# Kernel optimization log

Hardware: AMD Instinct MI355X
Metric: run time of the kernel (lower is better)

## Reference

```python
import jax, jax.numpy as jnp
import numpy as np

B, S, DM = 8, 1024, 1024
H, DH = 16, 64  # num_heads, per-head dim (q=k=v=r)
SCALE = 64 ** 1 / 2  # faithful to source: d_k**1/2 == d_k/2 == 32.0


def setup_inputs() -> dict:
    key = jax.random.key(0)
    ks = jax.random.split(key, 13)
    std = 1.0 / np.sqrt(DM)
    def lin(k):
        kw, kb = jax.random.split(k)
        W = jax.random.uniform(kw, (DM, H * DH), jnp.float32, -std, std)
        b = jax.random.uniform(kb, (H * DH,), jnp.float32, -std, std)
        return W, b
    Wq, bq = lin(ks[0]); Wk, bk = lin(ks[1]); Wv, bv = lin(ks[2]); Wr, br = lin(ks[3])
    Wo = jax.random.uniform(ks[4], (H * DH, DM), jnp.float32, -std, std)
    bo = jax.random.uniform(ks[5], (DM,), jnp.float32, -std, std)
    return {
        "value": jax.random.normal(ks[6], (B, S, DM), jnp.float32),
        "key": jax.random.normal(ks[7], (B, S, DM), jnp.float32),
        "query": jax.random.normal(ks[8], (B, S, DM), jnp.float32),
        "Wq": Wq, "bq": bq, "Wk": Wk, "bk": bk,
        "Wv": Wv, "bv": bv, "Wr": Wr, "br": br,
        "Wo": Wo, "bo": bo,
    }


def reference(value, key, query, Wq, bq, Wk, bk, Wv, bv, Wr, br, Wo, bo):
    b = query.shape[0]
    # projections -> [b, s, h, d] -> [b, h, s, d]
    q = (query @ Wq + bq).reshape(b, -1, H, DH).transpose(0, 2, 1, 3)
    k = (key @ Wk + bk).reshape(b, -1, H, DH).transpose(0, 2, 1, 3)
    v = (value @ Wv + bv).reshape(b, -1, H, DH).transpose(0, 2, 1, 3)
    r = (query @ Wr + br).reshape(b, -1, H, DH).transpose(0, 2, 1, 3)
    energy = jnp.einsum('bhid,bhjd->bhij', q, k)
    attn = jax.nn.softmax(energy / SCALE, axis=-1)
    ctx = jnp.einsum('bhjd,bhij->bhid', v, attn)
    gated = (ctx * r).transpose(0, 2, 1, 3)  # R-gating, back to [b, s, h, d]
    out = gated.reshape(b, -1, H * DH) @ Wo + bo
    return out
```

## Files before the change

### kernel.cpp

```cpp
#include <hip/hip_runtime.h>
#include <stdint.h>

#define B_ 8
#define S_ 1024
#define DM_ 1024
#define H_ 16
#define DH_ 64
#define M_ (B_*S_)

typedef unsigned short u16;
typedef unsigned int u32;
typedef __attribute__((ext_vector_type(8))) short bf16x8;
typedef __attribute__((ext_vector_type(4))) float f32x4;

__device__ __forceinline__ u16 f2bf(float f){
  union { float f; u32 u; } x; x.f = f;
  u32 r = x.u + 0x7fffu + ((x.u >> 16) & 1u);
  return (u16)(r >> 16);
}
__device__ __forceinline__ float bf2f(u16 u){
  union { u32 u; float f; } x; x.u = ((u32)u) << 16; return x.f;
}
__device__ __forceinline__ u32 cvtpk(float lo, float hi){
  u32 r; asm("v_cvt_pk_bf16_f32 %0, %1, %2" : "=v"(r) : "v"(lo), "v"(hi)); return r;
}
__device__ __forceinline__ void gload16(const void* g, void* l){
  __builtin_amdgcn_global_load_lds((const __attribute__((address_space(1))) void*)g,
                                   (__attribute__((address_space(3))) void*)l, 16, 0, 0);
}

__global__ void k_cvt_act(const float* __restrict__ v, const float* __restrict__ k,
                          const float* __restrict__ q, u16* __restrict__ vb,
                          u16* __restrict__ kb, u16* __restrict__ qb){
  int z = blockIdx.y;
  const float* src = (z == 0) ? v : (z == 1) ? k : q;
  u16* dst = (z == 0) ? vb : (z == 1) ? kb : qb;
  size_t i = ((size_t)blockIdx.x * blockDim.x + threadIdx.x) * 8;
  float4 a = *(const float4*)(src + i);
  float4 b = *(const float4*)(src + i + 4);
  uint4 o;
  o.x = (u32)f2bf(a.x) | ((u32)f2bf(a.y) << 16);
  o.y = (u32)f2bf(a.z) | ((u32)f2bf(a.w) << 16);
  o.z = (u32)f2bf(b.x) | ((u32)f2bf(b.y) << 16);
  o.w = (u32)f2bf(b.z) | ((u32)f2bf(b.w) << 16);
  *(uint4*)(dst + i) = o;
}

__global__ void k_cvt_wt(const float* __restrict__ w0, const float* __restrict__ w1,
                         const float* __restrict__ w2, const float* __restrict__ w3,
                         const float* __restrict__ w4,
                         u16* __restrict__ wall, u16* __restrict__ wot){
  __shared__ float tile[32][33];
  int z = blockIdx.z;
  const float* src = (z==0)?w0:(z==1)?w1:(z==2)?w2:(z==3)?w3:w4;
  u16* dst = (z<4) ? (wall + (size_t)z * 1048576) : wot;
  int n0 = blockIdx.x * 32, k0 = blockIdx.y * 32;
  int tx = threadIdx.x, ty = threadIdx.y;
#pragma unroll
  for (int i=0;i<4;i++) tile[ty+8*i][tx] = src[(size_t)(k0+ty+8*i)*DM_ + n0+tx];
  __syncthreads();
#pragma unroll
  for (int i=0;i<4;i++) dst[(size_t)(n0+ty+8*i)*DM_ + k0+tx] = f2bf(tile[tx][ty+8*i]);
}

__global__ __launch_bounds__(512, 2) void k_proj8(const u16* __restrict__ qb, const u16* __restrict__ kb,
                                                  const u16* __restrict__ vb, const u16* __restrict__ wall,
                                                  const float* __restrict__ bqp, const float* __restrict__ brp,
                                                  const float* __restrict__ bkp, const float* __restrict__ bvp,
                                                  u16* __restrict__ qpj, u16* __restrict__ rpj,
                                                  u16* __restrict__ kpj, u16* __restrict__ vtg){
  extern __shared__ u16 smem[];
  u16* As = smem;
  u16* Bs = smem + 32768;
  const int tid = threadIdx.x;
  const int w = tid >> 6, l = tid & 63, g = l >> 4, s = l & 15;
  const int wr = w >> 2, wc = w & 3;
  const int m0 = blockIdx.x << 8;
  const int ng0 = blockIdx.y << 8;
  const int chunk = ng0 >> 10;
  const u16* A = (chunk < 2) ? qb : (chunk == 2) ? kb : vb;

  u32 offA[2][2], offB[2][2];
#pragma unroll
  for (int h=0; h<2; h++)
#pragma unroll
    for (int i2=0; i2<2; i2++){
      int c = tid + i2*512; int rw = c >> 3, sl = c & 7;
      offA[h][i2] = (u32)((m0  + h*128 + rw) << 10) + ((sl ^ (rw & 7)) << 3);
      offB[h][i2] = (u32)((ng0 + h*128 + rw) << 10) + ((sl ^ (rw & 7)) << 3);
    }
  const u16* pA[2]; const u16* pB[2];
#pragma unroll
  for (int ks=0; ks<2; ks++){
    pA[ks] = &As[(wr*128 + s)*64 + (((ks*4+g) ^ (s & 7)) << 3)];
    pB[ks] = &Bs[(wc*64  + s)*64 + (((ks*4+g) ^ (s & 7)) << 3)];
  }

  f32x4 acc[8][4];
#pragma unroll
  for (int i=0;i<8;i++)
#pragma unroll
    for (int j=0;j<4;j++) acc[i][j] = (f32x4){0.f,0.f,0.f,0.f};

#define PSTAGE_A(buf, TCE, h) do { \
    gload16(Ak + offA[h][0] + (TCE), &As[(buf)*16384 + (h)*8192 + (w*64)*8]); \
    gload16(Ak + offA[h][1] + (TCE), &As[(buf)*16384 + (h)*8192 + (512 + w*64)*8]); \
  } while(0)

#define PSTAGE_B(buf, TCE, h) do { \
    gload16(Wk + offB[h][0] + (TCE), &Bs[(buf)*16384 + (h)*8192 + (w*64)*8]); \
    gload16(Wk + offB[h][1] + (TCE), &Bs[(buf)*16384 + (h)*8192 + (512 + w*64)*8]); \
  } while(0)

#define PLOADA(cb, mh) do { \
    _Pragma("unroll") for (int mi2=0; mi2<4; mi2++) \
    _Pragma("unroll") for (int ks=0; ks<2; ks++) \
      af[mi2][ks] = *(const bf16x8*)(pA[ks] + (cb)*16384 + (mh)*4096 + mi2*1024); \
    } while(0)

#define PLOADB(dst, cb, nh) do { \
    _Pragma("unroll") for (int ni2=0; ni2<2; ni2++) \
    _Pragma("unroll") for (int ks=0; ks<2; ks++) \
      dst[ni2][ks] = *(const bf16x8*)(pB[ks] + (cb)*16384 + (nh)*2048 + ni2*1024); \
    } while(0)

#define PMFMA(mh, nh, bfr) do { \
    _Pragma("unroll") for (int mi2=0; mi2<4; mi2++) \
    _Pragma("unroll") for (int ni2=0; ni2<2; ni2++) \
    _Pragma("unroll") for (int ks=0; ks<2; ks++) \
      acc[(mh)*4+mi2][(nh)*2+ni2] = __builtin_amdgcn_mfma_f32_16x16x32_bf16( \
          af[mi2][ks], bfr[ni2][ks], acc[(mh)*4+mi2][(nh)*2+ni2], 0, 0, 0); \
    } while(0)

#define BAR   __builtin_amdgcn_s_barrier()
#define PRIO1 __builtin_amdgcn_s_setprio(1)
#define PRIO0 __builtin_amdgcn_s_setprio(0)
#define VMC(N) asm volatile("s_waitcnt vmcnt(" #N ")" ::: "memory")

  {
    const u16* Ak = A;  const u16* Wk = wall;
    PSTAGE_A(0, 0, 0); PSTAGE_A(0, 0, 1); PSTAGE_B(0, 0, 0); PSTAGE_B(0, 0, 1);
    PSTAGE_B(1, 64, 0); PSTAGE_B(1, 64, 1);
  }
  VMC(4);
  BAR;

#pragma unroll 1
  for (int it = 0; it < 8; ++it){
    const u16* Ak = A + it*128;
    const u16* Wk = wall + it*128;
    const bool pre = (it < 7);
    {
      bf16x8 af[4][2], bf0[2][2], bf1[2][2];
      PSTAGE_A(1, 64, 0);
      PLOADA(0, 0); PLOADB(bf0, 0, 0);
      PRIO1; PMFMA(0, 0, bf0); PRIO0; BAR;
      PSTAGE_A(1, 64, 1);
      PLOADB(bf1, 0, 1);
      PRIO1; PMFMA(0, 1, bf1); PRIO0;
      VMC(8);
      BAR;
      if (pre) PSTAGE_B(0, 128, 0);
      PLOADA(0, 1);
      PRIO1; PMFMA(1, 1, bf1); PRIO0; BAR;
      if (pre) PSTAGE_B(0, 128, 1);
      PRIO1; PMFMA(1, 0, bf0); PRIO0;
      if (it == 7) VMC(0); else VMC(6);
      BAR;
    }
    {
      bf16x8 af[4][2], bf0[2][2], bf1[2][2];
      if (pre) PSTAGE_A(0, 128, 0);
      PLOADA(1, 0); PLOADB(bf0, 1, 0);
      PRIO1; PMFMA(0, 0, bf0); PRIO0; BAR;
      if (pre) PSTAGE_A(0, 128, 1);
      PLOADB(bf1, 1, 1);
      PRIO1; PMFMA(0, 1, bf1); PRIO0;
      VMC(8);
      BAR;
      if (pre) PSTAGE_B(1, 192, 0);
      PLOADA(1, 1);
      PRIO1; PMFMA(1, 1, bf1); PRIO0; BAR;
      if (pre) PSTAGE_B(1, 192, 1);
      PRIO1; PMFMA(1, 0, bf0); PRIO0;
      VMC(6);
      BAR;
    }
  }

  const float* bias = (chunk==0)?bqp:(chunk==1)?brp:(chunk==2)?bkp:bvp;
  u16* outp = (chunk==0)?qpj:(chunk==1)?rpj:kpj;
#pragma unroll
  for (int ni=0; ni<4; ni++){
    int cg = ng0 + wc*64 + ni*16 + s;
    int col = cg & 1023;
    float bv = bias[col];
#pragma unroll
    for (int mi=0; mi<8; mi++){
      int row = m0 + wr*128 + mi*16 + g*4;
      if (chunk == 3){
        union { short4 v; u16 e[4]; } pk2;
#pragma unroll
        for (int r=0;r<4;r++) pk2.e[r] = f2bf(acc[mi][ni][r] + bv);
        size_t vrow = ((size_t)(row >> 10) * 16 + (col >> 6)) * 64 + (col & 63);
        *(short4*)&vtg[(vrow << 10) + (row & 1023)] = pk2.v;
      } else {
#pragma unroll
        for (int r=0;r<4;r++)
          outp[((size_t)(row+r) << 10) + col] = f2bf(acc[mi][ni][r] + bv);
      }
    }
  }
#undef PSTAGE_A
#undef PSTAGE_B
#undef PLOADA
#undef PLOADB
#undef PMFMA
#undef BAR
#undef PRIO1
#undef PRIO0
#undef VMC
}

__global__ __launch_bounds__(256) void k_gemm_out(const u16* __restrict__ A, const u16* __restrict__ Bt,
                                                  const float* __restrict__ bias, float* __restrict__ Out){
  __shared__ u16 As[128*64];
  __shared__ u16 Bs[128*64];
  const int tid = threadIdx.x;
  const int w = tid >> 6, l = tid & 63, g = l >> 4, s = l & 15;
  const int wr = w >> 1, wc = w & 1;
  const int m0 = blockIdx.x << 7, n0 = blockIdx.y << 7;
  f32x4 acc[4][4];
#pragma unroll
  for (int i=0;i<4;i++)
#pragma unroll
    for (int j=0;j<4;j++) acc[i][j] = (f32x4){0.f,0.f,0.f,0.f};

  for (int k0 = 0; k0 < 1024; k0 += 64){
    __syncthreads();
#pragma unroll
    for (int i=0;i<4;i++){
      int c = tid + i*256;
      int m = c >> 3, slot = c & 7;
      gload16(A + ((size_t)(m0+m) << 10) + (k0 + ((slot ^ (m & 7)) << 3)),
              &As[(i*256 + w*64) * 8]);
    }
#pragma unroll
    for (int i=0;i<4;i++){
      int c = tid + i*256;
      int n = c >> 3, slot = c & 7;
      gload16(Bt + ((size_t)(n0+n) << 10) + (k0 + ((slot ^ (n & 7)) << 3)),
              &Bs[(i*256 + w*64) * 8]);
    }
    __syncthreads();
#pragma unroll
    for (int ks=0; ks<2; ks++){
      bf16x8 af[4], bfv[4];
#pragma unroll
      for (int mi=0;mi<4;mi++){
        int m = wr*64 + mi*16 + s;
        af[mi] = *(const bf16x8*)&As[m*64 + (((ks*4+g) ^ (s & 7)) << 3)];
      }
#pragma unroll
      for (int ni=0;ni<4;ni++){
        int n = wc*64 + ni*16 + s;
        bfv[ni] = *(const bf16x8*)&Bs[n*64 + (((ks*4+g) ^ (s & 7)) << 3)];
      }
#pragma unroll
      for (int mi=0;mi<4;mi++)
#pragma unroll
        for (int ni=0;ni<4;ni++)
          acc[mi][ni] = __builtin_amdgcn_mfma_f32_16x16x32_bf16(af[mi], bfv[ni], acc[mi][ni], 0, 0, 0);
    }
  }
#pragma unroll
  for (int ni=0;ni<4;ni++){
    int col = n0 + wc*64 + ni*16 + s;
    float bv = bias[col];
#pragma unroll
    for (int mi=0;mi<4;mi++){
      int row = m0 + wr*64 + mi*16 + g*4;
#pragma unroll
      for (int r=0;r<4;r++)
        Out[((size_t)(row+r) << 10) + col] = acc[mi][ni][r] + bv;
    }
  }
}

__global__ __launch_bounds__(512) void k_attn(const u16* __restrict__ qp, const u16* __restrict__ kp,
                                              const u16* __restrict__ vtg, const u16* __restrict__ rp,
                                              u16* __restrict__ gated){
  __shared__ u16 Ks[2][64*64];
  __shared__ u16 Vs[2][64*64];
  __shared__ u32 PsU[8*16*32];
  const int tid = threadIdx.x;
  const int w = tid >> 6, l = tid & 63, g = l >> 4, s = l & 15;
  const int bid = blockIdx.x;
  const int swz = (bid & 7) * 128 + (bid >> 3);
  const int bh = swz >> 3;
  const int q0 = (swz & 7) << 7;
  const int b = bh >> 4, h = bh & 15;
  const size_t base = ((size_t)b << 20);
  const int colh = h << 6;
  const float KL = 1.4426950408889634f / 32.0f;

  const size_t qoff = base + ((size_t)(q0 + w*16 + s) << 10) + colh;
  bf16x8 qf0 = *(const bf16x8*)(qp + qoff + g*8);
  bf16x8 qf1 = *(const bf16x8*)(qp + qoff + 32 + g*8);
  const size_t vbase = ((size_t)(b*16 + h)) << 16;

  u32* PsW = PsU + (w << 9);
  const int sx2 = s << 1;

  const int rr = tid >> 3, sl = tid & 7;
  const u32 koff = (u32)(rr << 10) + colh + ((sl ^ (rr & 7)) << 3);
  const u32 voff = (u32)(rr << 10) + ((sl ^ (rr & 7)) << 3);
  const u16* kbgl = kp + base;
  const u16* vbgl = vtg + vbase;

  float mrun = -1e30f, lsum = 0.f;
  f32x4 of[4];
#pragma unroll
  for (int d=0;d<4;d++) of[d] = (f32x4){0.f,0.f,0.f,0.f};

#define STAGE_KV(BUF, KV0) do { \
    gload16(kbgl + ((u32)(KV0) << 10) + koff, &Ks[BUF][(w*64)*8]); \
    gload16(vbgl + (KV0) + voff, &Vs[BUF][(w*64)*8]); \
  } while(0)

  STAGE_KV(0, 0);
  __syncthreads();

  int cur = 0;
  for (int t = 0; t < 16; t++){
    if (t < 15) STAGE_KV(cur ^ 1, (t+1) << 6);
    const u16* ksb = Ks[cur];
    const u16* vsb = Vs[cur];

    f32x4 e2[4];
#pragma unroll
    for (int sjf=0;sjf<4;sjf++){
      e2[sjf] = (f32x4){0.f,0.f,0.f,0.f};
      int sj = sjf*16 + s;
      bf16x8 kf0 = *(const bf16x8*)&ksb[sj*64 + ((g ^ (s & 7)) << 3)];
      e2[sjf] = __builtin_amdgcn_mfma_f32_16x16x32_bf16(kf0, qf0, e2[sjf], 0, 0, 0);
      bf16x8 kf1 = *(const bf16x8*)&ksb[sj*64 + (((4+g) ^ (s & 7)) << 3)];
      e2[sjf] = __builtin_amdgcn_mfma_f32_16x16x32_bf16(kf1, qf1, e2[sjf], 0, 0, 0);
    }
    float rm = fmaxf(fmaxf(e2[0][0], e2[0][1]), e2[0][2]);
    rm = fmaxf(fmaxf(rm, e2[0][3]), e2[1][0]);
    rm = fmaxf(fmaxf(rm, e2[1][1]), e2[1][2]);
    rm = fmaxf(fmaxf(rm, e2[1][3]), e2[2][0]);
    rm = fmaxf(fmaxf(rm, e2[2][1]), e2[2][2]);
    rm = fmaxf(fmaxf(rm, e2[2][3]), e2[3][0]);
    rm = fmaxf(fmaxf(rm, e2[3][1]), e2[3][2]);
    rm = fmaxf(rm, e2[3][3]);
    rm = fmaxf(rm, __shfl_xor(rm, 16, 64));
    rm = fmaxf(rm, __shfl_xor(rm, 32, 64));
    if (!__all(rm <= mrun + 177.0f)){
      float nm = fmaxf(mrun, rm);
      float alpha = __builtin_amdgcn_exp2f((mrun - nm) * KL);
      mrun = nm;
      lsum *= alpha;
      float ac[4];
#pragma unroll
      for (int r=0;r<4;r++) ac[r] = __shfl(alpha, g*4 + r, 64);
#pragma unroll
      for (int d=0; d<4; d++)
#pragma unroll
        for (int r=0;r<4;r++) of[d][r] *= ac[r];
    }

    const float mk = mrun * KL;
#pragma unroll
    for (int sjf=0;sjf<4;sjf++){
      float p0 = __builtin_amdgcn_exp2f(e2[sjf][0]*KL - mk);
      float p1 = __builtin_amdgcn_exp2f(e2[sjf][1]*KL - mk);
      float p2 = __builtin_amdgcn_exp2f(e2[sjf][2]*KL - mk);
      float p3 = __builtin_amdgcn_exp2f(e2[sjf][3]*KL - mk);
      lsum += (p0 + p1) + (p2 + p3);
      uint2 pk; pk.x = cvtpk(p0, p1); pk.y = cvtpk(p2, p3);
      int phys = (8*sjf + 2*g) ^ sx2;
      *reinterpret_cast<uint2*>(&PsW[(s << 5) + phys]) = pk;
    }
    union { u32 u[4]; bf16x8 v; } pa0, pa1;
    {
      uint2 r0 = *reinterpret_cast<const uint2*>(&PsW[(s << 5) + ((4*g    ) ^ sx2)]);
      uint2 r1 = *reinterpret_cast<const uint2*>(&PsW[(s << 5) + ((4*g + 2) ^ sx2)]);
      pa0.u[0] = r0.x; pa0.u[1] = r0.y; pa0.u[2] = r1.x; pa0.u[3] = r1.y;
      uint2 r2 = *reinterpret_cast<const uint2*>(&PsW[(s << 5) + ((16 + 4*g    ) ^ sx2)]);
      uint2 r3 = *reinterpret_cast<const uint2*>(&PsW[(s << 5) + ((16 + 4*g + 2) ^ sx2)]);
      pa1.u[0] = r2.x; pa1.u[1] = r2.y; pa1.u[2] = r3.x; pa1.u[3] = r3.y;
    }
#pragma unroll
    for (int df=0; df<4; df++){
      int d = df*16 + s;
      bf16x8 v0 = *(const bf16x8*)&vsb[d*64 + ((g ^ (s & 7)) << 3)];
      bf16x8 v1 = *(const bf16x8*)&vsb[d*64 + (((4+g) ^ (s & 7)) << 3)];
      of[df] = __builtin_amdgcn_mfma_f32_16x16x32_bf16(pa0.v, v0, of[df], 0, 0, 0);
      of[df] = __builtin_amdgcn_mfma_f32_16x16x32_bf16(pa1.v, v1, of[df], 0, 0, 0);
    }
    __syncthreads();
    cur ^= 1;
  }
#undef STAGE_KV

  lsum += __shfl_xor(lsum, 16, 64);
  lsum += __shfl_xor(lsum, 32, 64);
  float inv = 1.0f / lsum;
  float ic[4];
#pragma unroll
  for (int r=0;r<4;r++) ic[r] = __shfl(inv, g*4 + r, 64);
#pragma unroll
  for (int df=0; df<4; df++){
#pragma unroll
    for (int r=0;r<4;r++){
      size_t row = (size_t)(q0 + w*16 + g*4 + r);
      size_t idx = base + (row << 10) + colh + df*16 + s;
      float o = of[df][r] * ic[r];
      float rg = bf2f(rp[idx]);
      gated[idx] = f2bf(o * rg);
    }
  }
}

extern "C" void kernel_launch(void* const* d_in, const int* in_sizes, int n_in,
                              void* d_out, int out_size, void* d_ws, size_t ws_size,
                              hipStream_t stream){
  (void)in_sizes; (void)n_in; (void)out_size; (void)ws_size;
  const float* value = (const float*)d_in[0];
  const float* key   = (const float*)d_in[1];
  const float* query = (const float*)d_in[2];
  const float* Wq = (const float*)d_in[3];  const float* bq = (const float*)d_in[4];
  const float* Wk = (const float*)d_in[5];  const float* bk = (const float*)d_in[6];
  const float* Wv = (const float*)d_in[7];  const float* bv = (const float*)d_in[8];
  const float* Wr = (const float*)d_in[9];  const float* br = (const float*)d_in[10];
  const float* Wo = (const float*)d_in[11]; const float* bo = (const float*)d_in[12];

  char* ws = (char*)d_ws;
  const size_t MB = (size_t)1 << 20;
  u16* qb   = (u16*)(ws + 0*MB);
  u16* kb   = (u16*)(ws + 16*MB);
  u16* vb   = (u16*)(ws + 32*MB);
  u16* wall = (u16*)(ws + 48*MB);
  u16* wot  = (u16*)(ws + 56*MB);
  u16* qpj  = (u16*)(ws + 58*MB);
  u16* kpj  = (u16*)(ws + 74*MB);
  u16* vtg  = (u16*)(ws + 90*MB);
  u16* rpj  = (u16*)(ws + 106*MB);
  u16* gat  = qb;

  (void)hipFuncSetAttribute(reinterpret_cast<const void*>(&k_proj8),
                            hipFuncAttributeMaxDynamicSharedMemorySize, 131072);

  k_cvt_act<<<dim3(4096, 3), 256, 0, stream>>>(value, key, query, vb, kb, qb);
  k_cvt_wt<<<dim3(32, 32, 5), dim3(32, 8), 0, stream>>>(Wq, Wr, Wk, Wv, Wo, wall, wot);
  k_proj8<<<dim3(32, 16), 512, 131072, stream>>>(qb, kb, vb, wall, bq, br, bk, bv,
                                                 qpj, rpj, kpj, vtg);
  k_attn<<<1024, 512, 0, stream>>>(qpj, kpj, vtg, rpj, gat);
  k_gemm_out<<<dim3(64, 8), 256, 0, stream>>>(gat, wot, bo, (float*)d_out);
}
```

Measured before the change: 190.0 us.

## Software-pipeline LDS fragment loads ahead of MFMA phases in projection GEMM

Restructures the projection GEMM main loop so the LDS-to-register fragment loads for the next MFMA phase are issued before the current phase's MFMAs, using double sets of A/B fragment registers that persist across iterations. This is meant to hide LDS read latency behind matrix-core work instead of stalling on each load. It raises register pressure, which may reduce occupancy or cause spills, and it reorders waitcnt and barrier placement in a way that must stay correct against the global-to-LDS staging.

Measured after the change: 329.9 us. 1.74x slower.

```diff
diff --git a/kernel.cpp b/kernel.cpp
--- a/kernel.cpp
+++ b/kernel.cpp
@@ -112,10 +112,10 @@
     gload16(Wk + offB[h][1] + (TCE), &Bs[(buf)*16384 + (h)*8192 + (512 + w*64)*8]); \
   } while(0)
 
-#define PLOADA(cb, mh) do { \
+#define PLOADA(dst, cb, mh) do { \
     _Pragma("unroll") for (int mi2=0; mi2<4; mi2++) \
     _Pragma("unroll") for (int ks=0; ks<2; ks++) \
-      af[mi2][ks] = *(const bf16x8*)(pA[ks] + (cb)*16384 + (mh)*4096 + mi2*1024); \
+      dst[mi2][ks] = *(const bf16x8*)(pA[ks] + (cb)*16384 + (mh)*4096 + mi2*1024); \
     } while(0)
 
 #define PLOADB(dst, cb, nh) do { \
@@ -124,12 +124,12 @@
       dst[ni2][ks] = *(const bf16x8*)(pB[ks] + (cb)*16384 + (nh)*2048 + ni2*1024); \
     } while(0)
 
-#define PMFMA(mh, nh, bfr) do { \
+#define PMFMA(mh, nh, afr, bfr) do { \
     _Pragma("unroll") for (int mi2=0; mi2<4; mi2++) \
     _Pragma("unroll") for (int ni2=0; ni2<2; ni2++) \
     _Pragma("unroll") for (int ks=0; ks<2; ks++) \
       acc[(mh)*4+mi2][(nh)*2+ni2] = __builtin_amdgcn_mfma_f32_16x16x32_bf16( \
-          af[mi2][ks], bfr[ni2][ks], acc[(mh)*4+mi2][(nh)*2+ni2], 0, 0, 0); \
+          afr[mi2][ks], bfr[ni2][ks], acc[(mh)*4+mi2][(nh)*2+ni2], 0, 0, 0); \
     } while(0)
 
 #define BAR   __builtin_amdgcn_s_barrier()
@@ -137,6 +137,9 @@
 #define PRIO0 __builtin_amdgcn_s_setprio(0)
 #define VMC(N) asm volatile("s_waitcnt vmcnt(" #N ")" ::: "memory")
 
+  bf16x8 aX0[4][2], aX1[4][2], aY0[4][2], aY1[4][2];
+  bf16x8 bX0[2][2], bX1[2][2], bY0[2][2], bY1[2][2];
+
   {
     const u16* Ak = A;  const u16* Wk = wall;
     PSTAGE_A(0, 0, 0); PSTAGE_A(0, 0, 1); PSTAGE_B(0, 0, 0); PSTAGE_B(0, 0, 1);
@@ -144,48 +147,41 @@
   }
   VMC(4);
   BAR;
+  PLOADA(aX0, 0, 0); PLOADB(bX0, 0, 0);
 
 #pragma unroll 1
   for (int it = 0; it < 8; ++it){
     const u16* Ak = A + it*128;
     const u16* Wk = wall + it*128;
     const bool pre = (it < 7);
-    {
-      bf16x8 af[4][2], bf0[2][2], bf1[2][2];
-      PSTAGE_A(1, 64, 0);
-      PLOADA(0, 0); PLOADB(bf0, 0, 0);
-      PRIO1; PMFMA(0, 0, bf0); PRIO0; BAR;
-      PSTAGE_A(1, 64, 1);
-      PLOADB(bf1, 0, 1);
-      PRIO1; PMFMA(0, 1, bf1); PRIO0;
-      VMC(8);
-      BAR;
-      if (pre) PSTAGE_B(0, 128, 0);
-      PLOADA(0, 1);
-      PRIO1; PMFMA(1, 1, bf1); PRIO0; BAR;
-      if (pre) PSTAGE_B(0, 128, 1);
-      PRIO1; PMFMA(1, 0, bf0); PRIO0;
-      if (it == 7) VMC(0); else VMC(6);
-      BAR;
-    }
-    {
-      bf16x8 af[4][2], bf0[2][2], bf1[2][2];
-      if (pre) PSTAGE_A(0, 128, 0);
-      PLOADA(1, 0); PLOADB(bf0, 1, 0);
-      PRIO1; PMFMA(0, 0, bf0); PRIO0; BAR;
-      if (pre) PSTAGE_A(0, 128, 1);
-      PLOADB(bf1, 1, 1);
-      PRIO1; PMFMA(0, 1, bf1); PRIO0;
-      VMC(8);
-      BAR;
-      if (pre) PSTAGE_B(1, 192, 0);
-      PLOADA(1, 1);
-      PRIO1; PMFMA(1, 1, bf1); PRIO0; BAR;
-      if (pre) PSTAGE_B(1, 192, 1);
-      PRIO1; PMFMA(1, 0, bf0); PRIO0;
+    PSTAGE_A(1, 64, 0);
+    PLOADB(bX1, 0, 1);
+    PRIO1; PMFMA(0, 0, aX0, bX0); PRIO0; BAR;
+    PSTAGE_A(1, 64, 1);
+    VMC(8);
+    PLOADA(aX1, 0, 1);
+    PRIO1; PMFMA(0, 1, aX0, bX1); PRIO0; BAR;
+    if (pre) PSTAGE_B(0, 128, 0);
+    PRIO1; PMFMA(1, 1, aX1, bX1); PRIO0; BAR;
+    if (pre) PSTAGE_B(0, 128, 1);
+    if (it == 7) VMC(0); else VMC(6);
+    PLOADA(aY0, 1, 0); PLOADB(bY0, 1, 0);
+    PRIO1; PMFMA(1, 0, aX1, bX0); PRIO0; BAR;
+    if (pre) PSTAGE_A(0, 128, 0);
+    PLOADB(bY1, 1, 1);
+    PRIO1; PMFMA(0, 0, aY0, bY0); PRIO0; BAR;
+    if (pre) PSTAGE_A(0, 128, 1);
+    VMC(8);
+    PLOADA(aY1, 1, 1);
+    PRIO1; PMFMA(0, 1, aY0, bY1); PRIO0; BAR;
+    if (pre) PSTAGE_B(1, 192, 0);
+    PRIO1; PMFMA(1, 1, aY1, bY1); PRIO0; BAR;
+    if (pre) PSTAGE_B(1, 192, 1);
+    if (pre){
       VMC(6);
-      BAR;
-    }
+      PLOADA(aX0, 0, 0); PLOADB(bX0, 0, 0);
+    }
+    PRIO1; PMFMA(1, 0, aY1, bY0); PRIO0; BAR;
   }
 
   const float* bias = (chunk==0)?bqp:(chunk==1)?brp:(chunk==2)?bkp:bvp;
```
